# Performance work log

Hardware: AMD Instinct MI355X
Metric: run time of the kernel (lower is better)

## Reference

```python
import jax, jax.numpy as jnp
import numpy as np

N = 100000      # nodes
IN_DIM = 128    # input feature dim
HID = 64        # hidden_dim / out_dim per head
HEADS = 4
E_RAND = 1600000  # random edges; self-loops appended -> E = E_RAND + N
SCALES = 3


def setup_inputs() -> dict:
    key = jax.random.key(0)
    ks = jax.random.split(key, 12)
    h = jax.random.normal(ks[0], (N, IN_DIM), dtype=jnp.float32)
    src = jax.random.randint(ks[1], (E_RAND,), 0, N)
    dst = jax.random.randint(ks[2], (E_RAND,), 0, N)
    loop = jnp.arange(N)
    src = jnp.concatenate([src, loop])  # self-loops ensure every dst has a mailbox
    dst = jnp.concatenate([dst, loop])
    frac_cover_mat = jax.random.randint(ks[3], (N, SCALES), 0, N)
    # learned params (bias=False everywhere); xavier-ish scaling
    layer1_fc = jax.random.normal(ks[4], (HEADS, HID, IN_DIM), jnp.float32) / np.sqrt(IN_DIM)
    layer1_attn = jax.random.normal(ks[5], (HEADS, 2 * HID), jnp.float32) * 0.1
    layer2_fc = jax.random.normal(ks[6], (HID, HID * HEADS), jnp.float32) / np.sqrt(HID * HEADS)
    layer2_attn = jax.random.normal(ks[7], (2 * HID,), jnp.float32) * 0.1
    frac_w = jax.random.normal(ks[8], (SCALES, HID, IN_DIM), jnp.float32) / np.sqrt(IN_DIM)
    frac_final_w = jax.random.normal(ks[9], (HID, SCALES * HID), jnp.float32) / np.sqrt(SCALES * HID)
    fc2_w = jax.random.normal(ks[10], (HID, 2 * HID), jnp.float32) / np.sqrt(2 * HID)
    return {"h": h, "src": src, "dst": dst, "frac_cover_mat": frac_cover_mat,
            "layer1_fc": layer1_fc, "layer1_attn": layer1_attn,
            "layer2_fc": layer2_fc, "layer2_attn": layer2_attn,
            "frac_w": frac_w, "frac_final_w": frac_final_w, "fc2_w": fc2_w}


def _gat_layer(z, src, dst, attn_w, n):
    # attn(cat([z_src, z_dst])) == z_src @ a_src + z_dst @ a_dst  (bias-free Linear)
    d = z.shape[1]
    e = jax.nn.leaky_relu(z[src] @ attn_w[:d] + z[dst] @ attn_w[d:])  # [E]
    # segment softmax over incoming edges of each dst node
    m = jax.ops.segment_max(e, dst, num_segments=n)
    ex = jnp.exp(e - m[dst])
    denom = jax.ops.segment_sum(ex, dst, num_segments=n)
    alpha = ex / denom[dst]                                   # [E]
    return jax.ops.segment_sum(alpha[:, None] * z[src], dst, num_segments=n)  # [N, d]


def reference(h, src, dst, frac_cover_mat,
              layer1_fc, layer1_attn, layer2_fc, layer2_attn,
              frac_w, frac_final_w, fc2_w):
    n = h.shape[0]
    # layer1: multi-head GAT, merge='cat'
    heads = []
    for i in range(layer1_fc.shape[0]):
        z = h @ layer1_fc[i].T                                # [N, HID]
        heads.append(_gat_layer(z, src, dst, layer1_attn[i], n))
    h_nei = jax.nn.elu(jnp.concatenate(heads, axis=1))        # [N, HID*HEADS]
    # layer2: single-head GAT
    z2 = h_nei @ layer2_fc.T                                  # [N, HID]
    h_nei = _gat_layer(z2, src, dst, layer2_attn, n)          # [N, HID]
    # fractal layer (dropout = identity in eval)
    h_all = [h[frac_cover_mat[:, s]] @ frac_w[s].T for s in range(frac_w.shape[0])]
    h_frac = jnp.concatenate(h_all, axis=1) @ frac_final_w.T  # [N, HID]
    # fc2 on cat([h_nei, h_frac]); dropout identity
    h_global = jnp.concatenate([h_nei, h_frac], axis=1) @ fc2_w.T  # [N, HID]
    # AvgPooling over single graph -> [1, HID]
    return jnp.mean(h_global, axis=0, keepdims=True)
```

## Files before the change

kernel.cpp:

```cpp
#include <hip/hip_runtime.h>
#include <math.h>


#define CAP 128

typedef unsigned int  uint_t;
typedef unsigned short ushort_t;
typedef __attribute__((ext_vector_type(8))) short short8;
typedef __attribute__((ext_vector_type(4))) float floatx4;
typedef __attribute__((ext_vector_type(2))) float floatx2;

__device__ __forceinline__ float wred_sum(float v){
#pragma unroll
  for (int o = 1; o < 64; o <<= 1) v += __shfl_xor(v, o, 64);
  return v;
}
__device__ __forceinline__ float lrelu(float x){ return x >= 0.f ? x : 0.01f*x; }
__device__ __forceinline__ ushort_t f2b(float f){
  uint_t u = __float_as_uint(f);
  u = (u + 0x7FFFu + ((u >> 16) & 1u)) >> 16;
  return (ushort_t)u;
}
__device__ __forceinline__ float b2f_lo(uint_t w){ return __uint_as_float(w << 16); }
__device__ __forceinline__ float b2f_hi(uint_t w){ return __uint_as_float(w & 0xFFFF0000u); }

__device__ __forceinline__ void agg8(uint2 u, float4 al,
    floatx2& c00, floatx2& c01, floatx2& c10, floatx2& c11){
  floatx2 p0 = __builtin_amdgcn_cvt_pk_f32_fp8(u.x, false);
  floatx2 p1 = __builtin_amdgcn_cvt_pk_f32_fp8(u.x, true);
  floatx2 p2 = __builtin_amdgcn_cvt_pk_f32_fp8(u.y, false);
  floatx2 p3 = __builtin_amdgcn_cvt_pk_f32_fp8(u.y, true);
  floatx2 aXY = {al.x, al.y}, aZW = {al.z, al.w};
  c00 += aXY * p0;
  c01 += aZW * p1;
  c10 += aXY * p2;
  c11 += aZW * p3;
}

__global__ void k_prep(const float* __restrict__ W1, const float* __restrict__ W2,
                       const float* __restrict__ a1, const float* __restrict__ a2,
                       const int* __restrict__ dstI, int E,
                       const int* __restrict__ fcm, int N3, int* __restrict__ cnt,
                       ushort_t* __restrict__ w1bp, float* __restrict__ v2,
                       int* __restrict__ deg){
  __shared__ float v[8][128];
  const int bx = blockIdx.x, t = threadIdx.x;
  if (bx < 128){
    int idx = bx*256 + t;
    int j = idx & 7, lane = (idx >> 3) & 63, ks = (idx >> 9) & 3, tt = idx >> 11;
    int n = tt*16 + (lane & 15), k = ks*32 + (lane >> 4)*8 + j;
    int hh = tt >> 2, m = tt & 3;
    int pt = (m < 2) ? (hh*2 + m) : (8 + hh*2 + (m - 2));
    w1bp[((pt*4 + ks)*64 + lane)*8 + j] = f2b(W1[n*128 + k]);
  } else if (bx == 128){
    for (int o = t; o < 1024; o += 256){
      int col = o >> 7, k = o & 127, hh = col & 3, off = (col >> 2)*64;
      float s = 0.f;
      for (int n = 0; n < 64; n++) s += a1[hh*128 + off + n] * W1[(hh*64 + n)*128 + k];
      v[col][k] = s;
    }
    __syncthreads();
    for (int idx = t; idx < 2048; idx += 256){
      int j = idx & 7, lane = (idx >> 3) & 63, ks = idx >> 9;
      int col = lane & 15, k = ks*32 + (lane >> 4)*8 + j;
      w1bp[32768 + idx] = (col < 8) ? f2b(v[col][k]) : (ushort_t)0;
    }
  } else if (bx == 129){
    float s0 = 0.f, s1 = 0.f;
    for (int j = 0; j < 64; j++){
      float wjk = W2[j*256 + t];
      s0 += wjk * a2[j];
      s1 += wjk * a2[64 + j];
    }
    v2[t] = s0; v2[256 + t] = s1;
  } else {
    const int nb = gridDim.x - 130;
    for (int i = (bx-130)*256 + t; i < E; i += nb*256)
      atomicAdd(&deg[dstI[i]], 1);
    for (int i = (bx-130)*256 + t; i < N3; i += nb*256){
      int v3 = fcm[i];
      atomicAdd(&cnt[v3*3 + (i % 3)], 1);
    }
  }
}

__global__ __launch_bounds__(256) void k_scan1(const int* __restrict__ deg, int* __restrict__ part){
  __shared__ int tmp[256];
  int t = threadIdx.x;
  tmp[t] = deg[blockIdx.x*256 + t];
  __syncthreads();
  for (int off = 128; off > 0; off >>= 1){
    if (t < off) tmp[t] += tmp[t+off];
    __syncthreads();
  }
  if (t == 0) part[blockIdx.x] = tmp[0];
}
__global__ __launch_bounds__(512) void k_scan2(int* __restrict__ part, int B){
  __shared__ int tmp[512];
  int t = threadIdx.x;
  int v = (t < B) ? part[t] : 0;
  tmp[t] = v; __syncthreads();
  for (int off = 1; off < 512; off <<= 1){
    int x = (t >= off) ? tmp[t-off] : 0;
    __syncthreads();
    tmp[t] += x;
    __syncthreads();
  }
  if (t < B) part[t] = tmp[t] - v;
}
__global__ __launch_bounds__(256) void k_scan3(const int* __restrict__ deg, const int* __restrict__ part,
    int* __restrict__ rowptr, int* __restrict__ cursor){
  __shared__ int tmp[256];
  int t = threadIdx.x, i = blockIdx.x*256 + t;
  int v = deg[i];
  tmp[t] = v; __syncthreads();
  for (int off = 1; off < 256; off <<= 1){
    int x = (t >= off) ? tmp[t-off] : 0;
    __syncthreads();
    tmp[t] += x;
    __syncthreads();
  }
  int excl = tmp[t] - v + part[blockIdx.x];
  rowptr[i] = excl; cursor[i] = excl;
}

__global__ __launch_bounds__(512, 4) void k_mega(const float* __restrict__ h,
    const ushort_t* __restrict__ w1bp,
    uint_t* __restrict__ z8, float* __restrict__ s1s, float* __restrict__ s1d, int N,
    const int* __restrict__ srcI, const int* __restrict__ dstI,
    int* __restrict__ cursor, int* __restrict__ csr, int E,
    int Gg, int Gs, int G, int step,
    const int* __restrict__ cnt, float* __restrict__ accFrac)
{
  static __shared__ __align__(16) char smem[36864];
  const int tid = threadIdx.x;
  const int id = (int)(((unsigned long long)blockIdx.x * (unsigned)step) % (unsigned)G);
  if (id < Gg){
    ushort_t* ldsB = (ushort_t*)smem;
    const int wave = tid >> 6, lane = tid & 63;
    const int quad = lane >> 4, l16 = lane & 15;
    const int row0 = id*128 + wave*16;
    const bool act = row0 < N;
    const int ar = act ? ((row0 + l16 < N) ? (row0 + l16) : (N - 1)) : 0;
    short8 AHI[4], ALO[4];
    if (act){
#pragma unroll
      for (int ks = 0; ks < 4; ks++){
        const float* ap = &h[(size_t)ar*128 + ks*32 + quad*8];
        float4 v0 = *(const float4*)ap;
        float4 v1 = *(const float4*)(ap + 4);
        float vv[8] = {v0.x,v0.y,v0.z,v0.w,v1.x,v1.y,v1.z,v1.w};
#pragma unroll
        for (int j = 0; j < 8; j++){
          ushort_t hb = f2b(vv[j]);
          float hf = __uint_as_float((uint_t)hb << 16);
          AHI[ks][j] = (short)hb;
          ALO[ks][j] = (short)f2b(vv[j] - hf);
        }
      }
    }
#pragma unroll
    for (int half = 0; half < 2; half++){
      __syncthreads();
      {
        const int cnt4 = half ? 2304 : 2048;
        const uint4* src = (const uint4*)w1bp + (half ? 2048 : 0);
        uint4* dst = (uint4*)ldsB;
        for (int i = tid; i < cnt4; i += 512) dst[i] = src[i];
      }
      __syncthreads();
      if (!act) continue;
      const int nt = half ? 9 : 8;
      floatx4 c[9];
#pragma unroll
      for (int i = 0; i < 9; i++) c[i] = (floatx4){0.f,0.f,0.f,0.f};
#pragma unroll
      for (int ks = 0; ks < 4; ks++){
        for (int i = 0; i < nt; i++){
          short8 b = *(const short8*)&ldsB[(size_t)((i*4 + ks)*64 + lane)*8];
          c[i] = __builtin_amdgcn_mfma_f32_16x16x32_bf16(AHI[ks], b, c[i], 0, 0, 0);
        }
        if (half){
          short8 b = *(const short8*)&ldsB[(size_t)((8*4 + ks)*64 + lane)*8];
          c[8] = __builtin_amdgcn_mfma_f32_16x16x32_bf16(ALO[ks], b, c[8], 0, 0, 0);
        }
      }
      const int m0 = half ? 2 : 0;
#pragma unroll
      for (int i = 0; i < 4; i++){
        const int r = row0 + quad*4 + i;
        if (r >= N) continue;
#pragma unroll
        for (int dm = 0; dm < 2; dm++){
          int u = 0;
          u = __builtin_amdgcn_cvt_pk_fp8_f32(c[0*2+dm][i], c[1*2+dm][i], u, false);
          u = __builtin_amdgcn_cvt_pk_fp8_f32(c[2*2+dm][i], c[3*2+dm][i], u, true);
          z8[(size_t)r*64 + (m0+dm)*16 + l16] = (uint_t)u;
        }
        if (half){
          const float sv = c[8][i];
          if (l16 < 4) s1s[r*4 + l16] = sv;
          else if (l16 < 8) s1d[r*4 + (l16 - 4)] = sv;
        }
      }
    }
  } else if (id < Gg + Gs){
    const int i = (id - Gg)*512 + tid;
    if (i < E){
      int p = atomicAdd(&cursor[dstI[i]], 1);
      csr[p] = srcI[i];
    }
  } else {
    float (*red)[384] = (float(*)[384])smem;
    const int wave = tid >> 6, lane = tid & 63;
    const int g = lane >> 5, li = lane & 31;
    const int Gf = G - Gg - Gs;
    const int stream0 = (id - Gg - Gs)*16 + wave*2 + g;
    const int step16 = Gf * 16;
    float4 a0 = {0,0,0,0}, a1 = {0,0,0,0}, a2 = {0,0,0,0};
    for (int n = stream0; n < N; n += step16){
      const float w0 = (float)cnt[n*3];
      const float w1 = (float)cnt[n*3+1];
      const float w2 = (float)cnt[n*3+2];
      float4 v = *(const float4*)&h[(size_t)n*128 + li*4];
      a0.x += w0*v.x; a0.y += w0*v.y; a0.z += w0*v.z; a0.w += w0*v.w;
      a1.x += w1*v.x; a1.y += w1*v.y; a1.z += w1*v.z; a1.w += w1*v.w;
      a2.x += w2*v.x; a2.y += w2*v.y; a2.z += w2*v.z; a2.w += w2*v.w;
    }
    const int w16 = wave*2 + g;
    *(float4*)&red[w16][0*128 + li*4] = a0;
    *(float4*)&red[w16][1*128 + li*4] = a1;
    *(float4*)&red[w16][2*128 + li*4] = a2;
    __syncthreads();
    for (int i = tid; i < 384; i += 512){
      float v = 0.f;
#pragma unroll
      for (int w = 0; w < 16; w++) v += red[w][i];
      atomicAdd(&accFrac[i], v);
    }
  }
}

__global__ __launch_bounds__(256) void k_gat1(
    const uint_t* __restrict__ z8, const float* __restrict__ s1src, const float* __restrict__ s1dst,
    const int* __restrict__ rowptr, const int* __restrict__ csr, const float* __restrict__ v2,
    uint_t* __restrict__ hneib, float* __restrict__ s2s, float* __restrict__ s2d, int N, int dbase)
{
  __shared__ int   sbuf[4][CAP];
  __shared__ __align__(16) float4 ebuf[4][CAP];
  __shared__ float v2s[512];
  const int tid = threadIdx.x;
  v2s[tid] = v2[tid];
  v2s[tid + 256] = v2[tid + 256];
  __syncthreads();
  const int wave = tid >> 6, lane = tid & 63;
  const int dst = (dbase + blockIdx.x)*4 + wave;
  if (dst >= N) return;
  const int beg = rowptr[dst];
  const int deg = rowptr[dst+1] - beg;
  const float4 sd = *(const float4*)&s1dst[dst*4];
  float t0=0.f,t1=0.f,t2=0.f,t3=0.f;
  for (int j = lane; j < deg; j += 64){
    int s = csr[beg+j];
    float4 sv = *(const float4*)&s1src[s*4];
    float4 a;
    a.x = __expf(lrelu(sv.x+sd.x)); a.y = __expf(lrelu(sv.y+sd.y));
    a.z = __expf(lrelu(sv.z+sd.z)); a.w = __expf(lrelu(sv.w+sd.w));
    if (j < CAP){ sbuf[wave][j] = s*64; ebuf[wave][j] = a; }
    t0 += a.x; t1 += a.y; t2 += a.z; t3 += a.w;
  }
  const float inv[4] = {1.f/wred_sum(t0), 1.f/wred_sum(t1), 1.f/wred_sum(t2), 1.f/wred_sum(t3)};
  const int eh = lane >> 5, li = lane & 31;
  floatx2 c00 = {0.f,0.f}, c01 = {0.f,0.f}, c10 = {0.f,0.f}, c11 = {0.f,0.f};
  if (deg <= CAP){
    const int j0 = (eh < deg) ? eh : 0;
    int offc = sbuf[wave][j0];
    float4 alc = ebuf[wave][j0];
    uint2 uc = *((const uint2*)(z8 + offc) + li);
    for (int jj = 0; jj + 2 <= deg; jj += 2){
      const int jn = jj + 2 + eh;
      const int jnc = (jn < deg) ? jn : (jj + eh);
      const int offn = sbuf[wave][jnc];
      const float4 aln = ebuf[wave][jnc];
      const uint2 un = *((const uint2*)(z8 + offn) + li);
      agg8(uc, alc, c00, c01, c10, c11);
      uc = un; alc = aln;
    }
    if ((deg & 1) && eh == 0)
      agg8(uc, alc, c00, c01, c10, c11);
  } else {
    for (int jj = 0; jj < deg; jj += 2){
      const int j = jj + eh;
      const bool v = j < deg;
      const int jc = v ? j : jj;
      int off; float4 al;
      if (jc < CAP){ off = sbuf[wave][jc]; al = ebuf[wave][jc]; }
      else {
        int s = csr[beg+jc];
        off = s*64;
        float4 sv = *(const float4*)&s1src[s*4];
        al.x = __expf(lrelu(sv.x+sd.x)); al.y = __expf(lrelu(sv.y+sd.y));
        al.z = __expf(lrelu(sv.z+sd.z)); al.w = __expf(lrelu(sv.w+sd.w));
      }
      if (!v){ al.x=0.f; al.y=0.f; al.z=0.f; al.w=0.f; }
      uint2 u = *((const uint2*)(z8 + off) + li);
      agg8(u, al, c00, c01, c10, c11);
    }
  }
  float acc[2][4] = {{c00.x, c00.y, c01.x, c01.y},
                     {c10.x, c10.y, c11.x, c11.y}};
#pragma unroll
  for (int k = 0; k < 2; k++)
#pragma unroll
    for (int hh = 0; hh < 4; hh++) acc[k][hh] += __shfl_xor(acc[k][hh], 32, 64);
  const float* vv = &v2s[eh*256];
  float p = 0.f;
#pragma unroll
  for (int hh = 0; hh < 4; hh++){
    float e0 = acc[0][hh]*inv[hh]; e0 = e0 > 0.f ? e0 : expm1f(e0);
    float e1 = acc[1][hh]*inv[hh]; e1 = e1 > 0.f ? e1 : expm1f(e1);
    p += e0 * vv[hh*64 + 2*li] + e1 * vv[hh*64 + 2*li + 1];
    if ((hh >> 1) == eh)
      hneib[(size_t)dst*128 + hh*32 + li] = (uint_t)f2b(e0) | ((uint_t)f2b(e1) << 16);
  }
#pragma unroll
  for (int o = 1; o < 32; o <<= 1) p += __shfl_xor(p, o, 64);
  if (lane == 0)  s2s[dst] = p;
  if (lane == 32) s2d[dst] = p;
}

__global__ __launch_bounds__(256) void k_aw2(
    const float* __restrict__ s2s, const float* __restrict__ s2d,
    const int* __restrict__ rowptr, const int* __restrict__ csr,
    float* __restrict__ wsrc, int N)
{
  __shared__ int   sbuf[4][CAP];
  __shared__ float ebuf[4][CAP];
  const int wave = threadIdx.x >> 6, lane = threadIdx.x & 63;
  const int dst = blockIdx.x*4 + wave;
  if (dst >= N) return;
  const int beg = rowptr[dst], deg = rowptr[dst+1] - beg;
  const float sd = s2d[dst];
  float ts = 0.f;
  for (int j = lane; j < deg; j += 64){
    int s = csr[beg+j];
    float a = __expf(lrelu(s2s[s] + sd));
    if (j < CAP){ sbuf[wave][j] = s; ebuf[wave][j] = a; }
    ts += a;
  }
  const float inv = 1.f/wred_sum(ts);
  for (int j = lane; j < deg; j += 64){
    int s; float a;
    if (j < CAP){ s = sbuf[wave][j]; a = ebuf[wave][j]; }
    else { s = csr[beg+j]; a = __expf(lrelu(s2s[s] + sd)); }
    atomicAdd(&wsrc[s], a * inv);
  }
}

__global__ __launch_bounds__(256) void k_hsum(const uint_t* __restrict__ hneib,
    const float* __restrict__ wsrc, float* __restrict__ acc256, int N)
{
  __shared__ float pr[512];
  const int t = threadIdx.x;
  const int h2 = t >> 7, p = t & 127;
  float a0 = 0.f, a1 = 0.f;
  const int step = gridDim.x * 2;
  for (int n = blockIdx.x*2 + h2; n < N; n += step){
    float wn = wsrc[n];
    uint_t u = hneib[(size_t)n*128 + p];
    a0 += wn * b2f_lo(u);
    a1 += wn * b2f_hi(u);
  }
  pr[h2*256 + 2*p]     = a0;
  pr[h2*256 + 2*p + 1] = a1;
  __syncthreads();
  float v = pr[t] + pr[256 + t];
  int pp = t >> 1;
  int d = (pp >> 5)*64 + 2*(pp & 31) + (t & 1);
  atomicAdd(&acc256[d], v);
}

__global__ __launch_bounds__(256) void k_finalize(const float* __restrict__ acc256,
    const float* __restrict__ accFrac, const float* __restrict__ W2,
    const float* __restrict__ frw, const float* __restrict__ frf,
    const float* __restrict__ fc2, float* __restrict__ out, float invN)
{
  __shared__ float mh[256], nei[64], g[384], mm[192], hfrac[64];
  int t = threadIdx.x;
  mh[t] = acc256[t] * invN;
  for (int i = t; i < 384; i += 256) g[i] = accFrac[i] * invN;
  __syncthreads();
  if (t < 64){
    float s = 0.f;
    for (int k = 0; k < 256; k++) s += W2[t*256 + k] * mh[k];
    nei[t] = s;
  }
  for (int i = t; i < 192; i += 256){
    int s = i >> 6, d = i & 63;
    const float* w = frw + (size_t)(s*64 + d)*128;
    const float* gs = g + s*128;
    float sum = 0.f;
    for (int k = 0; k < 128; k++) sum += gs[k]*w[k];
    mm[i] = sum;
  }
  __syncthreads();
  if (t < 64){
    float s = 0.f;
    for (int k = 0; k < 192; k++) s += mm[k]*frf[t*192 + k];
    hfrac[t] = s;
  }
  __syncthreads();
  if (t < 64){
    float o = 0.f;
    for (int k = 0; k < 64; k++)
      o += fc2[t*128 + k]*nei[k] + fc2[t*128 + 64 + k]*hfrac[k];
    out[t] = o;
  }
}

extern "C" void kernel_launch(void* const* d_in, const int* in_sizes, int n_in,
                              void* d_out, int out_size, void* d_ws, size_t ws_size,
                              hipStream_t stream)
{
  const float* h    = (const float*)d_in[0];
  const int*   srcI = (const int*)  d_in[1];
  const int*   dstI = (const int*)  d_in[2];
  const int*   fcm  = (const int*)  d_in[3];
  const float* l1fc = (const float*)d_in[4];
  const float* l1at = (const float*)d_in[5];
  const float* l2fc = (const float*)d_in[6];
  const float* l2at = (const float*)d_in[7];
  const float* frw  = (const float*)d_in[8];
  const float* frf  = (const float*)d_in[9];
  const float* fc2  = (const float*)d_in[10];
  float* out = (float*)d_out;
  (void)n_in; (void)out_size; (void)ws_size;

  const int N = in_sizes[0] / 128;
  const int E = in_sizes[1];
  const int B = (N + 256) / 256;
  const int PAD = B * 256;

  char* w = (char*)d_ws;
  size_t off = 0;
  auto alloc = [&](size_t bytes) -> char* {
    char* p = w + off; off = (off + bytes + 255) & ~(size_t)255; return p;
  };
  uint_t* z8    = (uint_t*)alloc((size_t)N*64*4);
  uint_t* hneib = (uint_t*)alloc((size_t)N*128*4);
  float* s1s  = (float*)alloc((size_t)N*4*4);
  float* s1d  = (float*)alloc((size_t)N*4*4);
  float* s2s  = (float*)alloc((size_t)N*4);
  float* s2d  = (float*)alloc((size_t)N*4);
  int*   deg     = (int*)  alloc((size_t)PAD*4);
  int*   cnt     = (int*)  alloc((size_t)N*3*4);
  float* wsrc    = (float*)alloc((size_t)N*4);
  float* acc256  = (float*)alloc(256*4);
  float* accFrac = (float*)alloc(384*4);
  const size_t zbytes = (size_t)((char*)accFrac + 384*4 - (char*)deg);
  int*   rowptr = (int*)alloc((size_t)PAD*4);
  int*   cursor = (int*)alloc((size_t)PAD*4);
  int*   part   = (int*)alloc(512*4);
  int*   csr    = (int*)alloc((size_t)E*4);
  ushort_t* w1bp = (ushort_t*)alloc(34816*2);
  float* v2     = (float*)alloc(512*4);

  hipMemsetAsync(deg, 0, zbytes, stream);

  hipLaunchKernelGGL(k_prep,  dim3(130 + 512), dim3(256), 0, stream,
                     l1fc, l2fc, l1at, l2at, dstI, E, fcm, 3*N, cnt, w1bp, v2, deg);
  hipLaunchKernelGGL(k_scan1, dim3(B),   dim3(256), 0, stream, deg, part);
  hipLaunchKernelGGL(k_scan2, dim3(1),   dim3(512), 0, stream, part, B);
  hipLaunchKernelGGL(k_scan3, dim3(B),   dim3(256), 0, stream, deg, part, rowptr, cursor);

  const int Gg = (N + 127) / 128;
  const int Gs = (E + 511) / 512;
  const int Gf = 512;
  const int G  = Gg + Gs + Gf;
  int step = (int)(G * 0.618) | 1;
  auto gcd = [](int a, int b){ while (b){ int t = a % b; a = b; b = t; } return a; };
  while (gcd(step, G) != 1) step += 2;

  hipLaunchKernelGGL(k_mega,  dim3(G), dim3(512), 0, stream,
                     h, w1bp, z8, s1s, s1d, N,
                     srcI, dstI, cursor, csr, E, Gg, Gs, G, step,
                     cnt, accFrac);
  const int nb  = (N + 3) / 4;
  const int nb1 = nb / 2;
  hipLaunchKernelGGL(k_gat1,  dim3(nb1),      dim3(256), 0, stream,
                     z8, s1s, s1d, rowptr, csr, v2, hneib, s2s, s2d, N, 0);
  hipLaunchKernelGGL(k_gat1,  dim3(nb - nb1), dim3(256), 0, stream,
                     z8, s1s, s1d, rowptr, csr, v2, hneib, s2s, s2d, N, nb1);
  hipLaunchKernelGGL(k_aw2,   dim3(nb),       dim3(256), 0, stream,
                     s2s, s2d, rowptr, csr, wsrc, N);
  hipLaunchKernelGGL(k_hsum,  dim3(608),      dim3(256), 0, stream,
                     hneib, wsrc, acc256, N);
  hipLaunchKernelGGL(k_finalize, dim3(1),     dim3(256), 0, stream,
                     acc256, accFrac, l2fc, frw, frf, fc2, out, 1.0f/(float)N);
}
```

Measured before the change: 535.3 us.

## Build CSR and CSC via per-XCD degree counters and deterministic ranks

Degree counting now uses per-XCD counter arrays with workgroup-scope atomics that record each edge's rank, for both the destination and source sides. The scatter step then computes edge positions from prefix-summed per-XCD bases instead of a global atomic cursor, and also builds a source-side position map. The layer-2 weight accumulation replaces float atomicAdd on wsrc with writes into a CSC-ordered alpha array followed by a per-node segmented sum. This removes contended cross-XCD atomics, but adds extra scan work, more memory traffic for the rank and position arrays, and one more kernel launch.

```diff
diff --git a/kernel.cpp b/kernel.cpp
--- a/kernel.cpp
+++ b/kernel.cpp
@@ -10,6 +10,11 @@
 typedef __attribute__((ext_vector_type(4))) float floatx4;
 typedef __attribute__((ext_vector_type(2))) float floatx2;
 
+__device__ __forceinline__ unsigned xcc_id(){
+  unsigned x;
+  asm volatile("s_getreg_b32 %0, hwreg(HW_REG_XCC_ID)" : "=s"(x));
+  return x & 7u;
+}
 __device__ __forceinline__ float wred_sum(float v){
 #pragma unroll
   for (int o = 1; o < 64; o <<= 1) v += __shfl_xor(v, o, 64);
@@ -39,10 +44,11 @@
 
 __global__ void k_prep(const float* __restrict__ W1, const float* __restrict__ W2,
                        const float* __restrict__ a1, const float* __restrict__ a2,
-                       const int* __restrict__ dstI, int E,
+                       const int* __restrict__ dstI, const int* __restrict__ srcI, int E,
                        const int* __restrict__ fcm, int N3, int* __restrict__ cnt,
                        ushort_t* __restrict__ w1bp, float* __restrict__ v2,
-                       int* __restrict__ deg){
+                       int* __restrict__ deg8, int* __restrict__ rk,
+                       int* __restrict__ degS8, int* __restrict__ rkS, int PAD){
   __shared__ float v[8][128];
   const int bx = blockIdx.x, t = threadIdx.x;
   if (bx < 128){
@@ -75,8 +81,19 @@
     v2[t] = s0; v2[256 + t] = s1;
   } else {
     const int nb = gridDim.x - 130;
-    for (int i = (bx-130)*256 + t; i < E; i += nb*256)
-      atomicAdd(&deg[dstI[i]], 1);
+    const unsigned xcd = xcc_id();
+    int* myDeg  = deg8  + (size_t)xcd * PAD;
+    int* myDegS = degS8 + (size_t)xcd * PAD;
+    for (int i = (bx-130)*256 + t; i < E; i += nb*256){
+      int d = dstI[i];
+      int s = srcI[i];
+      int r  = __hip_atomic_fetch_add(&myDeg[d], 1, __ATOMIC_RELAXED,
+                                      __HIP_MEMORY_SCOPE_WORKGROUP);
+      int rs = __hip_atomic_fetch_add(&myDegS[s], 1, __ATOMIC_RELAXED,
+                                      __HIP_MEMORY_SCOPE_WORKGROUP);
+      rk[i]  = (int)((xcd << 28) | (unsigned)r);
+      rkS[i] = (int)((xcd << 28) | (unsigned)rs);
+    }
     for (int i = (bx-130)*256 + t; i < N3; i += nb*256){
       int v3 = fcm[i];
       atomicAdd(&cnt[v3*3 + (i % 3)], 1);
@@ -84,21 +101,32 @@
   }
 }
 
-__global__ __launch_bounds__(256) void k_scan1(const int* __restrict__ deg, int* __restrict__ part){
+__global__ __launch_bounds__(256) void k_scan1(const int* __restrict__ deg8,
+    const int* __restrict__ degS8, int* __restrict__ partD,
+    int* __restrict__ partS, int B, int PAD){
   __shared__ int tmp[256];
-  int t = threadIdx.x;
-  tmp[t] = deg[blockIdx.x*256 + t];
+  const int bx = blockIdx.x;
+  const bool srcSide = bx >= B;
+  const int* dp = srcSide ? degS8 : deg8;
+  int* pp = srcSide ? partS : partD;
+  const int row = srcSide ? (bx - B) : bx;
+  int t = threadIdx.x, i = row*256 + t;
+  int v = 0;
+#pragma unroll
+  for (int x = 0; x < 8; x++) v += dp[(size_t)x*PAD + i];
+  tmp[t] = v;
   __syncthreads();
   for (int off = 128; off > 0; off >>= 1){
     if (t < off) tmp[t] += tmp[t+off];
     __syncthreads();
   }
-  if (t == 0) part[blockIdx.x] = tmp[0];
-}
-__global__ __launch_bounds__(512) void k_scan2(int* __restrict__ part, int B){
+  if (t == 0) pp[row] = tmp[0];
+}
+__global__ __launch_bounds__(512) void k_scan2(int* __restrict__ partD,
+    int* __restrict__ partS, int B){
   __shared__ int tmp[512];
   int t = threadIdx.x;
-  int v = (t < B) ? part[t] : 0;
+  int v = (t < B) ? partD[t] : 0;
   tmp[t] = v; __syncthreads();
   for (int off = 1; off < 512; off <<= 1){
     int x = (t >= off) ? tmp[t-off] : 0;
@@ -106,13 +134,35 @@
     tmp[t] += x;
     __syncthreads();
   }
-  if (t < B) part[t] = tmp[t] - v;
-}
-__global__ __launch_bounds__(256) void k_scan3(const int* __restrict__ deg, const int* __restrict__ part,
-    int* __restrict__ rowptr, int* __restrict__ cursor){
+  if (t < B) partD[t] = tmp[t] - v;
+  __syncthreads();
+  int v2 = (t < B) ? partS[t] : 0;
+  tmp[t] = v2; __syncthreads();
+  for (int off = 1; off < 512; off <<= 1){
+    int x = (t >= off) ? tmp[t-off] : 0;
+    __syncthreads();
+    tmp[t] += x;
+    __syncthreads();
+  }
+  if (t < B) partS[t] = tmp[t] - v2;
+}
+__global__ __launch_bounds__(256) void k_scan3(const int* __restrict__ deg8,
+    const int* __restrict__ degS8,
+    const int* __restrict__ partD, const int* __restrict__ partS,
+    int* __restrict__ rowptr, int* __restrict__ rowptrS,
+    int* __restrict__ base8, int* __restrict__ baseS8, int B, int PAD){
   __shared__ int tmp[256];
-  int t = threadIdx.x, i = blockIdx.x*256 + t;
-  int v = deg[i];
+  const int bx = blockIdx.x;
+  const bool srcSide = bx >= B;
+  const int* dp = srcSide ? degS8 : deg8;
+  const int* pp = srcSide ? partS : partD;
+  int* rp = srcSide ? rowptrS : rowptr;
+  int* bp = srcSide ? baseS8 : base8;
+  const int row = srcSide ? (bx - B) : bx;
+  int t = threadIdx.x, i = row*256 + t;
+  int d8[8]; int v = 0;
+#pragma unroll
+  for (int x = 0; x < 8; x++){ d8[x] = dp[(size_t)x*PAD + i]; v += d8[x]; }
   tmp[t] = v; __syncthreads();
   for (int off = 1; off < 256; off <<= 1){
     int x = (t >= off) ? tmp[t-off] : 0;
@@ -120,15 +170,20 @@
     tmp[t] += x;
     __syncthreads();
   }
-  int excl = tmp[t] - v + part[blockIdx.x];
-  rowptr[i] = excl; cursor[i] = excl;
+  int excl = tmp[t] - v + pp[row];
+  rp[i] = excl;
+  int run = excl;
+#pragma unroll
+  for (int x = 0; x < 8; x++){ bp[(size_t)x*PAD + i] = run; run += d8[x]; }
 }
 
 __global__ __launch_bounds__(512, 4) void k_mega(const float* __restrict__ h,
     const ushort_t* __restrict__ w1bp,
     uint_t* __restrict__ z8, float* __restrict__ s1s, float* __restrict__ s1d, int N,
     const int* __restrict__ srcI, const int* __restrict__ dstI,
-    int* __restrict__ cursor, int* __restrict__ csr, int E,
+    const int* __restrict__ rk, const int* __restrict__ rkS,
+    const int* __restrict__ base8, const int* __restrict__ baseS8, int PAD,
+    int* __restrict__ csr, int* __restrict__ csrPos, int E,
     int Gg, int Gs, int G, int step,
     const int* __restrict__ cnt, float* __restrict__ accFrac)
 {
@@ -207,8 +262,14 @@
   } else if (id < Gg + Gs){
     const int i = (id - Gg)*512 + tid;
     if (i < E){
-      int p = atomicAdd(&cursor[dstI[i]], 1);
-      csr[p] = srcI[i];
+      const int d = dstI[i];
+      const int s = srcI[i];
+      const uint_t uD = (uint_t)rk[i];
+      const uint_t uS = (uint_t)rkS[i];
+      const int pD = base8 [(size_t)(uD >> 28)*PAD + d] + (int)(uD & 0x0FFFFFFFu);
+      const int pS = baseS8[(size_t)(uS >> 28)*PAD + s] + (int)(uS & 0x0FFFFFFFu);
+      csr[pD]    = s;
+      csrPos[pD] = pS;
     }
   } else {
     float (*red)[384] = (float(*)[384])smem;
@@ -332,7 +393,7 @@
 __global__ __launch_bounds__(256) void k_aw2(
     const float* __restrict__ s2s, const float* __restrict__ s2d,
     const int* __restrict__ rowptr, const int* __restrict__ csr,
-    float* __restrict__ wsrc, int N)
+    const int* __restrict__ csrPos, float* __restrict__ alphaCSC, int N)
 {
   __shared__ int   sbuf[4][CAP];
   __shared__ float ebuf[4][CAP];
@@ -350,11 +411,22 @@
   }
   const float inv = 1.f/wred_sum(ts);
   for (int j = lane; j < deg; j += 64){
-    int s; float a;
-    if (j < CAP){ s = sbuf[wave][j]; a = ebuf[wave][j]; }
-    else { s = csr[beg+j]; a = __expf(lrelu(s2s[s] + sd)); }
-    atomicAdd(&wsrc[s], a * inv);
-  }
+    float a;
+    if (j < CAP){ a = ebuf[wave][j]; }
+    else { int s = csr[beg+j]; a = __expf(lrelu(s2s[s] + sd)); }
+    alphaCSC[csrPos[beg+j]] = a * inv;
+  }
+}
+
+__global__ __launch_bounds__(256) void k_wsum(const float* __restrict__ alphaCSC,
+    const int* __restrict__ rowptrS, float* __restrict__ wsrc, int N)
+{
+  const int n = blockIdx.x*256 + threadIdx.x;
+  if (n >= N) return;
+  const int b = rowptrS[n], e = rowptrS[n+1];
+  float s = 0.f;
+  for (int k = b; k < e; k++) s += alphaCSC[k];
+  wsrc[n] = s;
 }
 
 __global__ __launch_bounds__(256) void k_hsum(const uint_t* __restrict__ hneib,
@@ -448,30 +520,41 @@
   };
   uint_t* z8    = (uint_t*)alloc((size_t)N*64*4);
   uint_t* hneib = (uint_t*)alloc((size_t)N*128*4);
+  int*    rk    = (int*)hneib;
+  int*    rkS   = rk + E;
   float* s1s  = (float*)alloc((size_t)N*4*4);
   float* s1d  = (float*)alloc((size_t)N*4*4);
   float* s2s  = (float*)alloc((size_t)N*4);
   float* s2d  = (float*)alloc((size_t)N*4);
-  int*   deg     = (int*)  alloc((size_t)PAD*4);
+  int*   deg8    = (int*)  alloc((size_t)8*PAD*4);
+  int*   degS8   = (int*)  alloc((size_t)8*PAD*4);
   int*   cnt     = (int*)  alloc((size_t)N*3*4);
-  float* wsrc    = (float*)alloc((size_t)N*4);
   float* acc256  = (float*)alloc(256*4);
   float* accFrac = (float*)alloc(384*4);
-  const size_t zbytes = (size_t)((char*)accFrac + 384*4 - (char*)deg);
-  int*   rowptr = (int*)alloc((size_t)PAD*4);
-  int*   cursor = (int*)alloc((size_t)PAD*4);
-  int*   part   = (int*)alloc(512*4);
-  int*   csr    = (int*)alloc((size_t)E*4);
+  const size_t zbytes = (size_t)((char*)accFrac + 384*4 - (char*)deg8);
+  int*   rowptr  = (int*)alloc((size_t)PAD*4);
+  int*   rowptrS = (int*)alloc((size_t)PAD*4);
+  int*   base8   = (int*)alloc((size_t)8*PAD*4);
+  int*   baseS8  = (int*)alloc((size_t)8*PAD*4);
+  int*   partD   = (int*)alloc(512*4);
+  int*   partS   = (int*)alloc(512*4);
+  int*   csr     = (int*)alloc((size_t)E*4);
+  int*   csrPos  = (int*)alloc((size_t)E*4);
+  float* alphaCSC= (float*)alloc((size_t)E*4);
+  float* wsrc    = (float*)alloc((size_t)N*4);
   ushort_t* w1bp = (ushort_t*)alloc(34816*2);
   float* v2     = (float*)alloc(512*4);
 
-  hipMemsetAsync(deg, 0, zbytes, stream);
+  hipMemsetAsync(deg8, 0, zbytes, stream);
 
   hipLaunchKernelGGL(k_prep,  dim3(130 + 512), dim3(256), 0, stream,
-                     l1fc, l2fc, l1at, l2at, dstI, E, fcm, 3*N, cnt, w1bp, v2, deg);
-  hipLaunchKernelGGL(k_scan1, dim3(B),   dim3(256), 0, stream, deg, part);
-  hipLaunchKernelGGL(k_scan2, dim3(1),   dim3(512), 0, stream, part, B);
-  hipLaunchKernelGGL(k_scan3, dim3(B),   dim3(256), 0, stream, deg, part, rowptr, cursor);
+                     l1fc, l2fc, l1at, l2at, dstI, srcI, E, fcm, 3*N, cnt, w1bp, v2,
+                     deg8, rk, degS8, rkS, PAD);
+  hipLaunchKernelGGL(k_scan1, dim3(2*B), dim3(256), 0, stream,
+                     deg8, degS8, partD, partS, B, PAD);
+  hipLaunchKernelGGL(k_scan2, dim3(1),   dim3(512), 0, stream, partD, partS, B);
+  hipLaunchKernelGGL(k_scan3, dim3(2*B), dim3(256), 0, stream,
+                     deg8, degS8, partD, partS, rowptr, rowptrS, base8, baseS8, B, PAD);
 
   const int Gg = (N + 127) / 128;
   const int Gs = (E + 511) / 512;
@@ -483,8 +566,8 @@
 
   hipLaunchKernelGGL(k_mega,  dim3(G), dim3(512), 0, stream,
                      h, w1bp, z8, s1s, s1d, N,
-                     srcI, dstI, cursor, csr, E, Gg, Gs, G, step,
-                     cnt, accFrac);
+                     srcI, dstI, rk, rkS, base8, baseS8, PAD, csr, csrPos, E,
+                     Gg, Gs, G, step, cnt, accFrac);
   const int nb  = (N + 3) / 4;
   const int nb1 = nb / 2;
   hipLaunchKernelGGL(k_gat1,  dim3(nb1),      dim3(256), 0, stream,
@@ -492,7 +575,9 @@
   hipLaunchKernelGGL(k_gat1,  dim3(nb - nb1), dim3(256), 0, stream,
                      z8, s1s, s1d, rowptr, csr, v2, hneib, s2s, s2d, N, nb1);
   hipLaunchKernelGGL(k_aw2,   dim3(nb),       dim3(256), 0, stream,
-                     s2s, s2d, rowptr, csr, wsrc, N);
+                     s2s, s2d, rowptr, csr, csrPos, alphaCSC, N);
+  hipLaunchKernelGGL(k_wsum,  dim3((N+255)/256), dim3(256), 0, stream,
+                     alphaCSC, rowptrS, wsrc, N);
   hipLaunchKernelGGL(k_hsum,  dim3(608),      dim3(256), 0, stream,
                      hneib, wsrc, acc256, N);
   hipLaunchKernelGGL(k_finalize, dim3(1),     dim3(256), 0, stream,
```

New measurement: 571.2 us. 6.7% more time.
